# Optimization experiments

Hardware: AMD Instinct MI355X
Metric: run time of the kernel (lower is better)

The kernel has to match this reference:

```python
import jax, jax.numpy as jnp
import numpy as np

NUM_HEADS = 16
HEAD_DIM = 128
HIDDEN = NUM_HEADS * HEAD_DIM


def rotate_half(x):
    x1, x2 = jnp.split(x, 2, axis=-1)
    return jnp.concatenate((-x2, x1), axis=-1)


def setup_inputs() -> dict:
    key = jax.random.key(0)
    ks = jax.random.split(key, 7)
    b, s = 2, 2048
    return {
        "hidden_states": jax.random.normal(ks[0], (b, s, HIDDEN), dtype=jnp.float32),
        "cos": jax.random.normal(ks[1], (1, 1, s, HEAD_DIM), dtype=jnp.float32),
        "sin": jax.random.normal(ks[2], (1, 1, s, HEAD_DIM), dtype=jnp.float32),
        "Wq": jax.random.normal(ks[3], (HIDDEN, HIDDEN), dtype=jnp.float32) * 0.02,
        "Wk": jax.random.normal(ks[4], (HIDDEN, HIDDEN), dtype=jnp.float32) * 0.02,
        "Wv": jax.random.normal(ks[5], (HIDDEN, HIDDEN), dtype=jnp.float32) * 0.02,
        "Wo": jax.random.normal(ks[6], (HIDDEN, HIDDEN), dtype=jnp.float32) * 0.02,
    }


def reference(hidden_states, cos, sin, Wq, Wk, Wv, Wo):
    b, s, _ = hidden_states.shape

    def proj(W):
        # [b,s,hidden] -> [b,H,s,D]
        return (hidden_states @ W).reshape(b, s, NUM_HEADS, HEAD_DIM).transpose(0, 2, 1, 3)

    q = proj(Wq)
    k = proj(Wk)
    v = proj(Wv)

    # RoPE: cos/sin [1,1,s,D] broadcast over batch and heads
    q = q * cos + rotate_half(q) * sin
    k = k * cos + rotate_half(k) * sin

    scale = 1.0 / jnp.sqrt(jnp.asarray(HEAD_DIM, dtype=q.dtype))
    scores = jnp.einsum("bhqd,bhkd->bhqk", q, k) * scale  # [b,H,s,s]
    attn = jax.nn.softmax(scores, axis=-1)  # no mask applied (matches source)
    out = jnp.einsum("bhqk,bhkd->bhqd", attn, v)  # [b,H,s,D]
    out = out.transpose(0, 2, 1, 3).reshape(b, s, HIDDEN)
    return out @ Wo
```

## Files before the change

kernel.cpp:

```cpp
#include <hip/hip_runtime.h>

typedef short bf16x8 __attribute__((ext_vector_type(8)));
typedef float f32x4 __attribute__((ext_vector_type(4)));

#define HID   2048
#define S_LEN 2048
#define NH    16
#define HD    128
#define BATCH 2
#define NROWS (BATCH * S_LEN)

__device__ __forceinline__ float bf2f(unsigned short u) {
    union { unsigned int i; float f; } v;
    v.i = ((unsigned int)u) << 16;
    return v.f;
}
__device__ __forceinline__ unsigned short f2bf(float f) {
    union { float f; unsigned int i; } v;
    v.f = f;
    unsigned int u = v.i;
    return (unsigned short)((u + 0x7fffu + ((u >> 16) & 1u)) >> 16);
}

__device__ __forceinline__ unsigned int pkbf(float a, float b) {
#if defined(__has_builtin) && __has_builtin(__builtin_amdgcn_cvt_pk_bf16_f32)
    typedef __bf16 bf2_t __attribute__((ext_vector_type(2)));
    bf2_t v = __builtin_amdgcn_cvt_pk_bf16_f32(a, b);
    unsigned int u;
    __builtin_memcpy(&u, &v, 4);
    return u;
#else
    return (unsigned int)f2bf(a) | ((unsigned int)f2bf(b) << 16);
#endif
}

__device__ __forceinline__ float exp2_fast(float x) {
#if defined(__has_builtin) && __has_builtin(__builtin_amdgcn_exp2f)
    return __builtin_amdgcn_exp2f(x);
#else
    return __expf(x * 0.6931471805599453f);
#endif
}

__device__ __forceinline__ void async16(const unsigned short* g, unsigned short* l) {
    __builtin_amdgcn_global_load_lds(
        (const __attribute__((address_space(1))) unsigned int*)g,
        (__attribute__((address_space(3))) unsigned int*)l, 16, 0, 0);
}

__global__ __launch_bounds__(256) void cast_f32_bf16(const float* __restrict__ x,
                                                     unsigned short* __restrict__ y, int n) {
    int i = (blockIdx.x * 256 + threadIdx.x) * 4;
    if (i < n) {
        float4 v = *(const float4*)(x + i);
        uint2 o;
        o.x = pkbf(v.x, v.y);
        o.y = pkbf(v.z, v.w);
        *(uint2*)(y + i) = o;
    }
}

__global__ __launch_bounds__(256) void merge_add(const float* __restrict__ a,
                                                 const float* __restrict__ b,
                                                 float* __restrict__ o, int n) {
    int i = (blockIdx.x * 256 + threadIdx.x) * 4;
    if (i < n) {
        float4 x = *(const float4*)(a + i);
        float4 y = *(const float4*)(b + i);
        x.x += y.x; x.y += y.y; x.z += y.z; x.w += y.w;
        *(float4*)(o + i) = x;
    }
}

__global__ __launch_bounds__(256) void transpose_cast(const float* __restrict__ Wa,
                                                      const float* __restrict__ Wb,
                                                      const float* __restrict__ Wc,
                                                      unsigned short* __restrict__ WT) {
    __shared__ float tile[32][33];
    int tx = threadIdx.x, ty = threadIdx.y;
    int bx = blockIdx.x, by = blockIdx.y, z = blockIdx.z;
    const float* W = (z == 0) ? Wa : ((z == 1) ? Wb : Wc);
    unsigned short* dst = WT + (size_t)z * HID * HID;
#pragma unroll
    for (int i = 0; i < 4; i++)
        tile[ty + i * 8][tx] = W[(size_t)(by * 32 + ty + i * 8) * HID + bx * 32 + tx];
    __syncthreads();
#pragma unroll
    for (int i = 0; i < 4; i++)
        dst[(size_t)(bx * 32 + ty + i * 8) * HID + by * 32 + tx] = f2bf(tile[tx][ty + i * 8]);
}

template <int MODE>
__global__ __launch_bounds__(256, 2) void gemm_bt(const unsigned short* __restrict__ A,
                                                  const unsigned short* __restrict__ Bt,
                                                  unsigned short* __restrict__ Qo,
                                                  unsigned short* __restrict__ Ko,
                                                  unsigned short* __restrict__ Vo,
                                                  float* __restrict__ Fo,
                                                  int n_shift, int kiters) {
    __shared__ unsigned short Asm[128 * 64];
    __shared__ unsigned short Bsm[128 * 64];
    int t = threadIdx.x;
    int wave = t >> 6, lane = t & 63;
    int wm = wave >> 1, wn = wave & 1;
    int c = lane & 15, quad = lane >> 4;
    int m0 = blockIdx.y * 128, nloc = blockIdx.x * 128;

    int lr = lane >> 3;
    int cb = (lane & 7) ^ (lr & 7);
    size_t kbase = (size_t)blockIdx.z * kiters * 64;
    const unsigned short* Ag = A + (size_t)(m0 + wave * 32 + lr) * HID + kbase + cb * 8;
    const unsigned short* Bg = Bt + (size_t)(nloc + wave * 32 + lr) * HID + kbase + cb * 8;
    unsigned short* Al = Asm + wave * 2048;
    unsigned short* Bl = Bsm + wave * 2048;

    f32x4 zero = {0.f, 0.f, 0.f, 0.f};
    f32x4 acc[4][4];
#pragma unroll
    for (int i = 0; i < 4; i++)
#pragma unroll
        for (int j = 0; j < 4; j++) acc[i][j] = zero;

    for (int it = 0; it < kiters; it++) {
        int k0 = it * 64;
#pragma unroll
        for (int j = 0; j < 4; j++) {
            async16(Ag + k0 + j * 8 * HID, Al + j * 512);
            async16(Bg + k0 + j * 8 * HID, Bl + j * 512);
        }
        __syncthreads();
#pragma unroll
        for (int kk = 0; kk < 2; kk++) {
            bf16x8 af[4], bfr[4];
#pragma unroll
            for (int mt = 0; mt < 4; mt++)
                af[mt] = *(const bf16x8*)(Asm + (wm * 64 + mt * 16 + c) * 64 +
                                          (((kk * 4 + quad) ^ (c & 7)) * 8));
#pragma unroll
            for (int nt = 0; nt < 4; nt++)
                bfr[nt] = *(const bf16x8*)(Bsm + (wn * 64 + nt * 16 + c) * 64 +
                                           (((kk * 4 + quad) ^ (c & 7)) * 8));
#pragma unroll
            for (int mt = 0; mt < 4; mt++)
#pragma unroll
                for (int nt = 0; nt < 4; nt++)
                    acc[mt][nt] = __builtin_amdgcn_mfma_f32_16x16x32_bf16(af[mt], bfr[nt],
                                                                          acc[mt][nt], 0, 0, 0);
        }
        __syncthreads();
    }

    if (MODE == 2) {
        float* Foz = Fo + (size_t)blockIdx.z * NROWS * HID;
#pragma unroll
        for (int mt = 0; mt < 4; mt++)
#pragma unroll
            for (int nt = 0; nt < 4; nt++)
#pragma unroll
                for (int r = 0; r < 4; r++) {
                    int row = m0 + wm * 64 + mt * 16 + quad * 4 + r;
                    int col = nloc + wn * 64 + nt * 16 + c;
                    Foz[(size_t)row * HID + col] = acc[mt][nt][r];
                }
    } else {
        int nglob0 = n_shift + nloc;
        int mat = nglob0 >> 11;
        int ncol0 = nglob0 & 2047;
        unsigned short* Cb = (mat == 0) ? Qo : ((mat == 1) ? Ko : Vo);
#pragma unroll
        for (int mt = 0; mt < 4; mt++) {
#pragma unroll
            for (int nt = 0; nt < 4; nt++) {
                int colm = ncol0 + wn * 64 + nt * 16 + c;
                int h = colm >> 7, d = colm & 127;
                if (mat < 2) {
#pragma unroll
                    for (int r = 0; r < 4; r++) {
                        int row = m0 + wm * 64 + mt * 16 + quad * 4 + r;
                        int b = row >> 11, s = row & 2047;
                        Cb[((size_t)(b * NH + h) * S_LEN + s) * HD + d] = f2bf(acc[mt][nt][r]);
                    }
                } else {
                    int row0 = m0 + wm * 64 + mt * 16 + quad * 4;
                    int b = row0 >> 11, s = row0 & 2047;
                    ushort4 o;
                    o.x = f2bf(acc[mt][nt][0]);
                    o.y = f2bf(acc[mt][nt][1]);
                    o.z = f2bf(acc[mt][nt][2]);
                    o.w = f2bf(acc[mt][nt][3]);
                    *(ushort4*)(Cb + ((size_t)(b * NH + h) * HD + d) * S_LEN + s) = o;
                }
            }
        }
    }
}

__global__ __launch_bounds__(256) void rope_kernel(unsigned short* __restrict__ Qb,
                                                   unsigned short* __restrict__ Kb,
                                                   const float* __restrict__ cosp,
                                                   const float* __restrict__ sinp) {
    unsigned short* P = blockIdx.y ? Kb : Qb;
    float scq = blockIdx.y ? 1.0f : 0.12751743f;
    int idx = blockIdx.x * 256 + threadIdx.x;
    int row = idx >> 6, j = idx & 63;
    int s = row & (S_LEN - 1);
    size_t base = (size_t)row * HD;
    float x1 = bf2f(P[base + j]);
    float x2 = bf2f(P[base + j + 64]);
    float c1 = cosp[s * HD + j], s1 = sinp[s * HD + j];
    float c2 = cosp[s * HD + j + 64], s2 = sinp[s * HD + j + 64];
    P[base + j]      = f2bf((x1 * c1 - x2 * s1) * scq);
    P[base + j + 64] = f2bf((x2 * c2 + x1 * s2) * scq);
}

#define PKS 72
__global__ __launch_bounds__(256, 2) void attn_kernel(const unsigned short* __restrict__ Q,
                                                      const unsigned short* __restrict__ Kg,
                                                      const unsigned short* __restrict__ Vt,
                                                      unsigned short* __restrict__ Aout) {
    __shared__ unsigned short Ksm[64 * 128];
    __shared__ unsigned short Vsm[128 * 64];
    __shared__ __align__(16) unsigned short Psm[4 * 2 * 16 * PKS];
    int bh = blockIdx.y;
    int b = bh >> 4, h = bh & 15;
    int t = threadIdx.x;
    int wave = t >> 6, lane = t & 63;
    int c = lane & 15, quad = lane >> 4;
    int q0 = blockIdx.x * 128 + wave * 32;
    const unsigned short* Qp = Q + (size_t)bh * S_LEN * HD;
    const unsigned short* Kp = Kg + (size_t)bh * S_LEN * HD;
    const unsigned short* Vp = Vt + (size_t)bh * HD * S_LEN;

    bf16x8 qf[2][4];
#pragma unroll
    for (int qn = 0; qn < 2; qn++)
#pragma unroll
        for (int kk = 0; kk < 4; kk++)
            qf[qn][kk] = *(const bf16x8*)(Qp + (size_t)(q0 + qn * 16 + c) * HD + kk * 32 + quad * 8);

    f32x4 zero = {0.f, 0.f, 0.f, 0.f};
    f32x4 o_acc[2][8];
#pragma unroll
    for (int qn = 0; qn < 2; qn++)
#pragma unroll
        for (int nt = 0; nt < 8; nt++) o_acc[qn][nt] = zero;
    float lsum[2] = {0.f, 0.f};

    for (int key0 = 0; key0 < S_LEN; key0 += 64) {
#pragma unroll
        for (int j = 0; j < 4; j++) {
            int fc = (wave * 4 + j) * 64 + lane;
            int rK = fc >> 4, cbK = (fc & 15) ^ (rK & 15);
            async16(Kp + (size_t)(key0 + rK) * HD + cbK * 8, Ksm + (wave * 4 + j) * 512);
            int rV = fc >> 3, cbV = (fc & 7) ^ (rV & 7);
            async16(Vp + (size_t)rV * S_LEN + key0 + cbV * 8, Vsm + (wave * 4 + j) * 512);
        }
        __syncthreads();

        f32x4 sacc[4][2];
#pragma unroll
        for (int km = 0; km < 4; km++)
#pragma unroll
            for (int qn = 0; qn < 2; qn++) sacc[km][qn] = zero;
#pragma unroll
        for (int kk = 0; kk < 4; kk++) {
            bf16x8 kfr[4];
#pragma unroll
            for (int km = 0; km < 4; km++)
                kfr[km] = *(const bf16x8*)(Ksm + (km * 16 + c) * HD + (((kk * 4 + quad) ^ c)) * 8);
#pragma unroll
            for (int km = 0; km < 4; km++)
#pragma unroll
                for (int qn = 0; qn < 2; qn++)
                    sacc[km][qn] = __builtin_amdgcn_mfma_f32_16x16x32_bf16(kfr[km], qf[qn][kk],
                                                                           sacc[km][qn], 0, 0, 0);
        }

#pragma unroll
        for (int qn = 0; qn < 2; qn++) {
#pragma unroll
            for (int km = 0; km < 4; km++) {
                float e0 = exp2_fast(sacc[km][qn][0]);
                float e1 = exp2_fast(sacc[km][qn][1]);
                float e2 = exp2_fast(sacc[km][qn][2]);
                float e3 = exp2_fast(sacc[km][qn][3]);
                lsum[qn] += (e0 + e1) + (e2 + e3);
                uint2 pk;
                pk.x = pkbf(e0, e1);
                pk.y = pkbf(e2, e3);
                *(uint2*)(Psm + ((wave * 2 + qn) * 16 + c) * PKS + km * 16 + quad * 4) = pk;
            }
        }
        asm volatile("" ::: "memory");
        __builtin_amdgcn_s_waitcnt(0xc07f);
        asm volatile("" ::: "memory");

#pragma unroll
        for (int kf = 0; kf < 2; kf++) {
            bf16x8 pf[2];
#pragma unroll
            for (int qn = 0; qn < 2; qn++)
                pf[qn] = *(const bf16x8*)(Psm + ((wave * 2 + qn) * 16 + c) * PKS + kf * 32 + quad * 8);
#pragma unroll
            for (int nt = 0; nt < 8; nt++) {
                bf16x8 vf = *(const bf16x8*)(Vsm + (nt * 16 + c) * 64 +
                                             (((kf * 4 + quad) ^ (c & 7))) * 8);
#pragma unroll
                for (int qn = 0; qn < 2; qn++)
                    o_acc[qn][nt] = __builtin_amdgcn_mfma_f32_16x16x32_bf16(pf[qn], vf,
                                                                            o_acc[qn][nt], 0, 0, 0);
            }
        }
        __syncthreads();
    }

#pragma unroll
    for (int qn = 0; qn < 2; qn++) {
        lsum[qn] += __shfl_xor(lsum[qn], 16);
        lsum[qn] += __shfl_xor(lsum[qn], 32);
    }
    float inv[2][4];
#pragma unroll
    for (int qn = 0; qn < 2; qn++)
#pragma unroll
        for (int r = 0; r < 4; r++)
            inv[qn][r] = 1.0f / __shfl(lsum[qn], quad * 4 + r);

#pragma unroll
    for (int qn = 0; qn < 2; qn++) {
#pragma unroll
        for (int r = 0; r < 4; r++) {
            int srow = q0 + qn * 16 + quad * 4 + r;
            size_t base = ((size_t)(b * S_LEN + srow)) * HID + h * HD;
#pragma unroll
            for (int nt = 0; nt < 8; nt++)
                Aout[base + nt * 16 + c] = f2bf(o_acc[qn][nt][r] * inv[qn][r]);
        }
    }
}

extern "C" void kernel_launch(void* const* d_in, const int* in_sizes, int n_in,
                              void* d_out, int out_size, void* d_ws, size_t ws_size,
                              hipStream_t stream) {
    const float* hs   = (const float*)d_in[0];
    const float* cosp = (const float*)d_in[1];
    const float* sinp = (const float*)d_in[2];
    const float* Wq   = (const float*)d_in[3];
    const float* Wk   = (const float*)d_in[4];
    const float* Wv   = (const float*)d_in[5];
    const float* Wo   = (const float*)d_in[6];

    char* ws = (char*)d_ws;
    unsigned short* Xb = (unsigned short*)(ws);
    unsigned short* Qb = (unsigned short*)(ws + (16ull << 20));
    unsigned short* Kb = (unsigned short*)(ws + (32ull << 20));
    unsigned short* Vb = (unsigned short*)(ws + (48ull << 20));
    unsigned short* WT = (unsigned short*)(ws + (64ull << 20));

    const bool fused = ws_size >= (88ull << 20);

    dim3 tb(32, 8);

    cast_f32_bf16<<<8192, 256, 0, stream>>>(hs, Xb, NROWS * HID);

    if (fused) {
        transpose_cast<<<dim3(64, 64, 3), tb, 0, stream>>>(Wq, Wk, Wv, WT);
        gemm_bt<0><<<dim3(48, 32, 1), 256, 0, stream>>>(Xb, WT, Qb, Kb, Vb, nullptr, 0, 32);
    } else {
        transpose_cast<<<dim3(64, 64, 1), tb, 0, stream>>>(Wq, Wq, Wq, WT);
        gemm_bt<0><<<dim3(16, 32, 1), 256, 0, stream>>>(Xb, WT, Qb, Kb, Vb, nullptr, 0, 32);
        transpose_cast<<<dim3(64, 64, 1), tb, 0, stream>>>(Wk, Wk, Wk, WT);
        gemm_bt<0><<<dim3(16, 32, 1), 256, 0, stream>>>(Xb, WT, Qb, Kb, Vb, nullptr, 2048, 32);
        transpose_cast<<<dim3(64, 64, 1), tb, 0, stream>>>(Wv, Wv, Wv, WT);
        gemm_bt<0><<<dim3(16, 32, 1), 256, 0, stream>>>(Xb, WT, Qb, Kb, Vb, nullptr, 4096, 32);
    }

    rope_kernel<<<dim3(16384, 2), 256, 0, stream>>>(Qb, Kb, cosp, sinp);

    attn_kernel<<<dim3(16, 32), 256, 0, stream>>>(Qb, Kb, Vb, Xb );

    if (fused) {
        unsigned short* WoT = (unsigned short*)(ws + (16ull << 20));
        float* Pf = (float*)(ws + (24ull << 20));
        transpose_cast<<<dim3(64, 64, 1), tb, 0, stream>>>(Wo, Wo, Wo, WoT);
        gemm_bt<2><<<dim3(16, 32, 2), 256, 0, stream>>>(Xb, WoT, nullptr, nullptr, nullptr,
                                                        Pf, 0, 16);
        merge_add<<<8192, 256, 0, stream>>>(Pf, Pf + (size_t)NROWS * HID, (float*)d_out,
                                            NROWS * HID);
    } else {
        transpose_cast<<<dim3(64, 64, 1), tb, 0, stream>>>(Wo, Wo, Wo, WT);
        gemm_bt<2><<<dim3(16, 32, 1), 256, 0, stream>>>(Xb, WT, nullptr, nullptr, nullptr,
                                                        (float*)d_out, 0, 32);
    }
}
```

Measured before the change: 417.1 us.

## Fuse RoPE into QKV GEMM epilogue, merge prep kernels, drop split-K output GEMM

The hidden-state cast and the QKV weight transpose now run as one prep launch. RoPE and the query scale are applied in the QKV GEMM epilogue by swapping half-tiles between partner waves through shared memory, which removes the separate rope kernel's read-modify-write pass over Q and K. The output projection drops split-K and the merge_add pass and writes directly to the output, trading fewer launches and less fp32 traffic for lower parallelism in that GEMM. RoPE now works from bf16-rounded partner values and adds two block barriers to the epilogue.

```diff
diff --git a/kernel.cpp b/kernel.cpp
--- a/kernel.cpp
+++ b/kernel.cpp
@@ -48,37 +48,29 @@
         (__attribute__((address_space(3))) unsigned int*)l, 16, 0, 0);
 }
 
-__global__ __launch_bounds__(256) void cast_f32_bf16(const float* __restrict__ x,
-                                                     unsigned short* __restrict__ y, int n) {
-    int i = (blockIdx.x * 256 + threadIdx.x) * 4;
-    if (i < n) {
-        float4 v = *(const float4*)(x + i);
-        uint2 o;
-        o.x = pkbf(v.x, v.y);
-        o.y = pkbf(v.z, v.w);
-        *(uint2*)(y + i) = o;
-    }
-}
-
-__global__ __launch_bounds__(256) void merge_add(const float* __restrict__ a,
-                                                 const float* __restrict__ b,
-                                                 float* __restrict__ o, int n) {
-    int i = (blockIdx.x * 256 + threadIdx.x) * 4;
-    if (i < n) {
-        float4 x = *(const float4*)(a + i);
-        float4 y = *(const float4*)(b + i);
-        x.x += y.x; x.y += y.y; x.z += y.z; x.w += y.w;
-        *(float4*)(o + i) = x;
-    }
-}
-
-__global__ __launch_bounds__(256) void transpose_cast(const float* __restrict__ Wa,
-                                                      const float* __restrict__ Wb,
-                                                      const float* __restrict__ Wc,
-                                                      unsigned short* __restrict__ WT) {
+__global__ __launch_bounds__(256) void prep(const float* __restrict__ hs,
+                                            const float* __restrict__ Wa,
+                                            const float* __restrict__ Wb,
+                                            const float* __restrict__ Wc,
+                                            unsigned short* __restrict__ Xb,
+                                            unsigned short* __restrict__ WT) {
+    int z = blockIdx.z;
+    int t = threadIdx.x;
+    if (z == 3) {
+        size_t idx = (((size_t)blockIdx.y * 64 + blockIdx.x) * 256 + t) * 8;
+        float4 v0 = *(const float4*)(hs + idx);
+        float4 v1 = *(const float4*)(hs + idx + 4);
+        uint4 o;
+        o.x = pkbf(v0.x, v0.y);
+        o.y = pkbf(v0.z, v0.w);
+        o.z = pkbf(v1.x, v1.y);
+        o.w = pkbf(v1.z, v1.w);
+        *(uint4*)(Xb + idx) = o;
+        return;
+    }
     __shared__ float tile[32][33];
-    int tx = threadIdx.x, ty = threadIdx.y;
-    int bx = blockIdx.x, by = blockIdx.y, z = blockIdx.z;
+    int tx = t & 31, ty = t >> 5;
+    int bx = blockIdx.x, by = blockIdx.y;
     const float* W = (z == 0) ? Wa : ((z == 1) ? Wb : Wc);
     unsigned short* dst = WT + (size_t)z * HID * HID;
 #pragma unroll
@@ -88,6 +80,21 @@
 #pragma unroll
     for (int i = 0; i < 4; i++)
         dst[(size_t)(bx * 32 + ty + i * 8) * HID + by * 32 + tx] = f2bf(tile[tx][ty + i * 8]);
+}
+
+__global__ __launch_bounds__(256) void transpose_cast(const float* __restrict__ W,
+                                                      unsigned short* __restrict__ WT) {
+    __shared__ float tile[32][33];
+    int t = threadIdx.x;
+    int tx = t & 31, ty = t >> 5;
+    int bx = blockIdx.x, by = blockIdx.y;
+#pragma unroll
+    for (int i = 0; i < 4; i++)
+        tile[ty + i * 8][tx] = W[(size_t)(by * 32 + ty + i * 8) * HID + bx * 32 + tx];
+    __syncthreads();
+#pragma unroll
+    for (int i = 0; i < 4; i++)
+        WT[(size_t)(bx * 32 + ty + i * 8) * HID + by * 32 + tx] = f2bf(tile[tx][ty + i * 8]);
 }
 
 template <int MODE>
@@ -97,9 +104,12 @@
                                                   unsigned short* __restrict__ Ko,
                                                   unsigned short* __restrict__ Vo,
                                                   float* __restrict__ Fo,
-                                                  int n_shift, int kiters) {
-    __shared__ unsigned short Asm[128 * 64];
-    __shared__ unsigned short Bsm[128 * 64];
+                                                  const float* __restrict__ cosp,
+                                                  const float* __restrict__ sinp,
+                                                  int n_shift) {
+    __shared__ unsigned short SM[16384];
+    unsigned short* Asm = SM;
+    unsigned short* Bsm = SM + 8192;
     int t = threadIdx.x;
     int wave = t >> 6, lane = t & 63;
     int wm = wave >> 1, wn = wave & 1;
@@ -108,9 +118,8 @@
 
     int lr = lane >> 3;
     int cb = (lane & 7) ^ (lr & 7);
-    size_t kbase = (size_t)blockIdx.z * kiters * 64;
-    const unsigned short* Ag = A + (size_t)(m0 + wave * 32 + lr) * HID + kbase + cb * 8;
-    const unsigned short* Bg = Bt + (size_t)(nloc + wave * 32 + lr) * HID + kbase + cb * 8;
+    const unsigned short* Ag = A + (size_t)(m0 + wave * 32 + lr) * HID + cb * 8;
+    const unsigned short* Bg = Bt + (size_t)(nloc + wave * 32 + lr) * HID + cb * 8;
     unsigned short* Al = Asm + wave * 2048;
     unsigned short* Bl = Bsm + wave * 2048;
 
@@ -121,7 +130,7 @@
 #pragma unroll
         for (int j = 0; j < 4; j++) acc[i][j] = zero;
 
-    for (int it = 0; it < kiters; it++) {
+    for (int it = 0; it < 32; it++) {
         int k0 = it * 64;
 #pragma unroll
         for (int j = 0; j < 4; j++) {
@@ -151,7 +160,6 @@
     }
 
     if (MODE == 2) {
-        float* Foz = Fo + (size_t)blockIdx.z * NROWS * HID;
 #pragma unroll
         for (int mt = 0; mt < 4; mt++)
 #pragma unroll
@@ -160,27 +168,18 @@
                 for (int r = 0; r < 4; r++) {
                     int row = m0 + wm * 64 + mt * 16 + quad * 4 + r;
                     int col = nloc + wn * 64 + nt * 16 + c;
-                    Foz[(size_t)row * HID + col] = acc[mt][nt][r];
+                    Fo[(size_t)row * HID + col] = acc[mt][nt][r];
                 }
     } else {
         int nglob0 = n_shift + nloc;
         int mat = nglob0 >> 11;
-        int ncol0 = nglob0 & 2047;
-        unsigned short* Cb = (mat == 0) ? Qo : ((mat == 1) ? Ko : Vo);
-#pragma unroll
-        for (int mt = 0; mt < 4; mt++) {
-#pragma unroll
-            for (int nt = 0; nt < 4; nt++) {
-                int colm = ncol0 + wn * 64 + nt * 16 + c;
-                int h = colm >> 7, d = colm & 127;
-                if (mat < 2) {
-#pragma unroll
-                    for (int r = 0; r < 4; r++) {
-                        int row = m0 + wm * 64 + mt * 16 + quad * 4 + r;
-                        int b = row >> 11, s = row & 2047;
-                        Cb[((size_t)(b * NH + h) * S_LEN + s) * HD + d] = f2bf(acc[mt][nt][r]);
-                    }
-                } else {
+        int h = (nglob0 & 2047) >> 7;
+        if (mat == 2) {
+#pragma unroll
+            for (int mt = 0; mt < 4; mt++)
+#pragma unroll
+                for (int nt = 0; nt < 4; nt++) {
+                    int d = wn * 64 + nt * 16 + c;
                     int row0 = m0 + wm * 64 + mt * 16 + quad * 4;
                     int b = row0 >> 11, s = row0 & 2047;
                     ushort4 o;
@@ -188,29 +187,45 @@
                     o.y = f2bf(acc[mt][nt][1]);
                     o.z = f2bf(acc[mt][nt][2]);
                     o.w = f2bf(acc[mt][nt][3]);
-                    *(ushort4*)(Cb + ((size_t)(b * NH + h) * HD + d) * S_LEN + s) = o;
+                    *(ushort4*)(Vo + ((size_t)(b * NH + h) * HD + d) * S_LEN + s) = o;
+                }
+        } else {
+            unsigned short* Cb = (mat == 0) ? Qo : Ko;
+            float scl = (mat == 0) ? 0.12751743f : 1.0f;
+            __syncthreads();
+#pragma unroll
+            for (int mt = 0; mt < 4; mt++)
+#pragma unroll
+                for (int nt = 0; nt < 4; nt++) {
+                    ushort4 o;
+                    o.x = f2bf(acc[mt][nt][0]);
+                    o.y = f2bf(acc[mt][nt][1]);
+                    o.z = f2bf(acc[mt][nt][2]);
+                    o.w = f2bf(acc[mt][nt][3]);
+                    *(ushort4*)(SM + (mt * 4 + nt) * 1024 + t * 4) = o;
+                }
+            __syncthreads();
+            int partner = (wm * 2 + (wn ^ 1)) * 64 + lane;
+            float sgn = wn ? 1.0f : -1.0f;
+#pragma unroll
+            for (int mt = 0; mt < 4; mt++) {
+#pragma unroll
+                for (int nt = 0; nt < 4; nt++) {
+                    ushort4 pv = *(const ushort4*)(SM + (mt * 4 + nt) * 1024 + partner * 4);
+                    float part[4] = {bf2f(pv.x), bf2f(pv.y), bf2f(pv.z), bf2f(pv.w)};
+                    int col = wn * 64 + nt * 16 + c;
+#pragma unroll
+                    for (int r = 0; r < 4; r++) {
+                        int row = m0 + wm * 64 + mt * 16 + quad * 4 + r;
+                        int b = row >> 11, s = row & 2047;
+                        float cv = cosp[s * HD + col], sv = sinp[s * HD + col];
+                        float out = (acc[mt][nt][r] * cv + sgn * part[r] * sv) * scl;
+                        Cb[((size_t)(b * NH + h) * S_LEN + s) * HD + col] = f2bf(out);
+                    }
                 }
             }
         }
     }
-}
-
-__global__ __launch_bounds__(256) void rope_kernel(unsigned short* __restrict__ Qb,
-                                                   unsigned short* __restrict__ Kb,
-                                                   const float* __restrict__ cosp,
-                                                   const float* __restrict__ sinp) {
-    unsigned short* P = blockIdx.y ? Kb : Qb;
-    float scq = blockIdx.y ? 1.0f : 0.12751743f;
-    int idx = blockIdx.x * 256 + threadIdx.x;
-    int row = idx >> 6, j = idx & 63;
-    int s = row & (S_LEN - 1);
-    size_t base = (size_t)row * HD;
-    float x1 = bf2f(P[base + j]);
-    float x2 = bf2f(P[base + j + 64]);
-    float c1 = cosp[s * HD + j], s1 = sinp[s * HD + j];
-    float c2 = cosp[s * HD + j + 64], s2 = sinp[s * HD + j + 64];
-    P[base + j]      = f2bf((x1 * c1 - x2 * s1) * scq);
-    P[base + j + 64] = f2bf((x2 * c2 + x1 * s2) * scq);
 }
 
 #define PKS 72
@@ -359,37 +374,29 @@
 
     const bool fused = ws_size >= (88ull << 20);
 
-    dim3 tb(32, 8);
-
-    cast_f32_bf16<<<8192, 256, 0, stream>>>(hs, Xb, NROWS * HID);
-
     if (fused) {
-        transpose_cast<<<dim3(64, 64, 3), tb, 0, stream>>>(Wq, Wk, Wv, WT);
-        gemm_bt<0><<<dim3(48, 32, 1), 256, 0, stream>>>(Xb, WT, Qb, Kb, Vb, nullptr, 0, 32);
+        prep<<<dim3(64, 64, 4), 256, 0, stream>>>(hs, Wq, Wk, Wv, Xb, WT);
+        gemm_bt<0><<<dim3(48, 32), 256, 0, stream>>>(Xb, WT, Qb, Kb, Vb, nullptr,
+                                                     cosp, sinp, 0);
+        attn_kernel<<<dim3(16, 32), 256, 0, stream>>>(Qb, Kb, Vb, Xb );
+        unsigned short* WoT = (unsigned short*)(ws + (16ull << 20));
+        transpose_cast<<<dim3(64, 64), 256, 0, stream>>>(Wo, WoT);
+        gemm_bt<2><<<dim3(16, 32), 256, 0, stream>>>(Xb, WoT, nullptr, nullptr, nullptr,
+                                                     (float*)d_out, cosp, sinp, 0);
     } else {
-        transpose_cast<<<dim3(64, 64, 1), tb, 0, stream>>>(Wq, Wq, Wq, WT);
-        gemm_bt<0><<<dim3(16, 32, 1), 256, 0, stream>>>(Xb, WT, Qb, Kb, Vb, nullptr, 0, 32);
-        transpose_cast<<<dim3(64, 64, 1), tb, 0, stream>>>(Wk, Wk, Wk, WT);
-        gemm_bt<0><<<dim3(16, 32, 1), 256, 0, stream>>>(Xb, WT, Qb, Kb, Vb, nullptr, 2048, 32);
-        transpose_cast<<<dim3(64, 64, 1), tb, 0, stream>>>(Wv, Wv, Wv, WT);
-        gemm_bt<0><<<dim3(16, 32, 1), 256, 0, stream>>>(Xb, WT, Qb, Kb, Vb, nullptr, 4096, 32);
-    }
-
-    rope_kernel<<<dim3(16384, 2), 256, 0, stream>>>(Qb, Kb, cosp, sinp);
-
-    attn_kernel<<<dim3(16, 32), 256, 0, stream>>>(Qb, Kb, Vb, Xb );
-
-    if (fused) {
-        unsigned short* WoT = (unsigned short*)(ws + (16ull << 20));
-        float* Pf = (float*)(ws + (24ull << 20));
-        transpose_cast<<<dim3(64, 64, 1), tb, 0, stream>>>(Wo, Wo, Wo, WoT);
-        gemm_bt<2><<<dim3(16, 32, 2), 256, 0, stream>>>(Xb, WoT, nullptr, nullptr, nullptr,
-                                                        Pf, 0, 16);
-        merge_add<<<8192, 256, 0, stream>>>(Pf, Pf + (size_t)NROWS * HID, (float*)d_out,
-                                            NROWS * HID);
-    } else {
-        transpose_cast<<<dim3(64, 64, 1), tb, 0, stream>>>(Wo, Wo, Wo, WT);
-        gemm_bt<2><<<dim3(16, 32, 1), 256, 0, stream>>>(Xb, WT, nullptr, nullptr, nullptr,
-                                                        (float*)d_out, 0, 32);
-    }
-}
+        prep<<<dim3(64, 64, 1), 256, 0, stream>>>(hs, Wq, Wq, Wq, Xb, WT);
+        prep<<<dim3(64, 64, 4), 256, 0, stream>>>(hs, Wq, Wq, Wq, Xb, WT);
+        gemm_bt<0><<<dim3(16, 32), 256, 0, stream>>>(Xb, WT, Qb, Kb, Vb, nullptr,
+                                                     cosp, sinp, 0);
+        transpose_cast<<<dim3(64, 64), 256, 0, stream>>>(Wk, WT);
+        gemm_bt<0><<<dim3(16, 32), 256, 0, stream>>>(Xb, WT, Qb, Kb, Vb, nullptr,
+                                                     cosp, sinp, 2048);
+        transpose_cast<<<dim3(64, 64), 256, 0, stream>>>(Wv, WT);
+        gemm_bt<0><<<dim3(16, 32), 256, 0, stream>>>(Xb, WT, Qb, Kb, Vb, nullptr,
+                                                     cosp, sinp, 4096);
+        attn_kernel<<<dim3(16, 32), 256, 0, stream>>>(Qb, Kb, Vb, Xb );
+        transpose_cast<<<dim3(64, 64), 256, 0, stream>>>(Wo, WT);
+        gemm_bt<2><<<dim3(16, 32), 256, 0, stream>>>(Xb, WT, nullptr, nullptr, nullptr,
+                                                     (float*)d_out, cosp, sinp, 0);
+    }
+}
```

Measured after the change: 396.7 us. -4.9%, faster.
